# Kernel tuning notes

Measured on AMD Instinct MI355X. Metric: run time of the kernel, lower is better.

## Reference

```python
import jax, jax.numpy as jnp
import numpy as np

EPS = 1e-5

def _conv1x1(x, w, b):
    # x: [B,C,H,W], w: [O,C], b: [O]  (1x1 conv == channel matmul)
    return jnp.einsum('bchw,oc->bohw', x, w) + b[None, :, None, None]

def _bn_relu(y, gamma, beta, mean, var):
    inv = gamma / jnp.sqrt(var + EPS)
    return jax.nn.relu(y * inv[None, :, None, None] + (beta - mean * inv)[None, :, None, None])

def setup_inputs() -> dict:
    key = jax.random.key(0)
    ks = jax.random.split(key, 8)
    B, C, H, W = 8, 2048, 48, 48
    mid = C // 4  # k = 4 -> mid_ch = 512
    s_in = (2.0 / C) ** 0.5   # kaiming-like scale for 1x1 convs from C channels
    s_mid = (2.0 / mid) ** 0.5
    return {
        'x': jax.random.normal(ks[0], (B, C, H, W), jnp.float32),
        'f_w': jax.random.normal(ks[1], (mid, C), jnp.float32) * s_in,
        'f_b': jnp.zeros((mid,), jnp.float32),
        'f_gamma': jnp.ones((mid,), jnp.float32),
        'f_beta': jnp.zeros((mid,), jnp.float32),
        'f_mean': jnp.zeros((mid,), jnp.float32),
        'f_var': jnp.ones((mid,), jnp.float32),
        'g_w': jax.random.normal(ks[2], (mid, C), jnp.float32) * s_in,
        'g_b': jnp.zeros((mid,), jnp.float32),
        'g_gamma': jnp.ones((mid,), jnp.float32),
        'g_beta': jnp.zeros((mid,), jnp.float32),
        'g_mean': jnp.zeros((mid,), jnp.float32),
        'g_var': jnp.ones((mid,), jnp.float32),
        'h_w': jax.random.normal(ks[3], (mid, C), jnp.float32) * s_in,
        'h_b': jnp.zeros((mid,), jnp.float32),
        'v_w': jax.random.normal(ks[4], (C, mid), jnp.float32) * s_mid,
        'v_b': jnp.zeros((C,), jnp.float32),
    }

def reference(x, f_w, f_b, f_gamma, f_beta, f_mean, f_var,
              g_w, g_b, g_gamma, g_beta, g_mean, g_var,
              h_w, h_b, v_w, v_b):
    B, C, H, W = x.shape
    mid = f_w.shape[0]
    N = H * W
    f_x = _bn_relu(_conv1x1(x, f_w, f_b), f_gamma, f_beta, f_mean, f_var).reshape(B, mid, N)
    g_x = _bn_relu(_conv1x1(x, g_w, g_b), g_gamma, g_beta, g_mean, g_var).reshape(B, mid, N)
    h_x = _conv1x1(x, h_w, h_b).reshape(B, mid, N)
    # z = f_x^T @ g_x : [B, N, N]
    scores = jnp.einsum('bcn,bcm->bnm', f_x, g_x) * (mid ** -0.5)
    attn = jax.nn.softmax(scores, axis=-1)
    # z = attn @ h_x^T : [B, N, mid] -> [B, mid, H, W]
    z = jnp.einsum('bnm,bcm->bcn', attn, h_x).reshape(B, mid, H, W)
    z = jnp.einsum('bchw,oc->bohw', z, v_w) + v_b[None, :, None, None]
    return (z + x, attn)
```

## Files before the change

### kernel.cpp

```cpp
#include <hip/hip_runtime.h>
#include <math.h>

typedef unsigned short u16;
typedef unsigned short u16x8 __attribute__((ext_vector_type(8)));
typedef __bf16 bf16x8 __attribute__((ext_vector_type(8)));
typedef float f32x4 __attribute__((ext_vector_type(4)));

typedef __attribute__((address_space(1))) const unsigned int gu32;
typedef __attribute__((address_space(3))) unsigned int su32;

#define B_ 8
#define C_ 2048
#define MID_ 512
#define N_ 2304

#define BAR() do { asm volatile("" ::: "memory"); __builtin_amdgcn_s_barrier(); asm volatile("" ::: "memory"); } while (0)

#define QMFMA(AV, BV, MO, NO)                                                             \
  { _Pragma("unroll") for (int mfi = 0; mfi < 4; ++mfi) {                                 \
      _Pragma("unroll") for (int nfi = 0; nfi < 2; ++nfi) {                               \
        acc[MO + mfi][NO + nfi] = __builtin_amdgcn_mfma_f32_16x16x32_bf16(                \
            AV[0][mfi], BV[0][nfi], acc[MO + mfi][NO + nfi], 0, 0, 0);                    \
        acc[MO + mfi][NO + nfi] = __builtin_amdgcn_mfma_f32_16x16x32_bf16(                \
            AV[1][mfi], BV[1][nfi], acc[MO + mfi][NO + nfi], 0, 0, 0); } } }

static __device__ __forceinline__ u16 f2bf(float f) {
  union { float f; unsigned u; } c; c.f = f;
  unsigned u = c.u;
  u += 0x7fffu + ((u >> 16) & 1u);
  return (u16)(u >> 16);
}
static __device__ __forceinline__ float bf2f(u16 x) {
  union { unsigned u; float f; } c; c.u = ((unsigned)x) << 16; return c.f;
}

__global__ __launch_bounds__(256) void prep_wall_k(
    const float* __restrict__ fw, const float* __restrict__ gw,
    const float* __restrict__ hw, u16* __restrict__ wall) {
  int idx = blockIdx.x * 256 + threadIdx.x;
  if (idx >= 1536 * 2048) return;
  int r = idx >> 11;
  float v = (r < 512) ? fw[idx] : (r < 1024) ? gw[idx - (512 << 11)] : hw[idx - (1024 << 11)];
  wall[idx] = f2bf(v);
}

__global__ __launch_bounds__(256) void prep_vw_k(const float* __restrict__ vw, u16* __restrict__ o) {
  int idx = blockIdx.x * 256 + threadIdx.x;
  if (idx < 2048 * 512) o[idx] = f2bf(vw[idx]);
}

__global__ __launch_bounds__(256) void prep_sb_k(
    const float* fb, const float* fg, const float* fbe, const float* fm, const float* fv,
    const float* gb, const float* gg, const float* gbe, const float* gm, const float* gv,
    const float* hb, float* __restrict__ scale, float* __restrict__ bias) {
  int i = blockIdx.x * 256 + threadIdx.x;
  if (i >= 1536) return;
  const float FS = 0.044194173824159216f;
  if (i < 512) {
    float inv = fg[i] / sqrtf(fv[i] + 1e-5f);
    scale[i] = inv * FS; bias[i] = (fb[i] * inv + fbe[i] - fm[i] * inv) * FS;
  } else if (i < 1024) {
    int j = i - 512;
    float inv = gg[j] / sqrtf(gv[j] + 1e-5f);
    scale[i] = inv; bias[i] = gb[j] * inv + gbe[j] - gm[j] * inv;
  } else {
    scale[i] = 1.0f; bias[i] = hb[i - 1024];
  }
}

__global__ __launch_bounds__(256) void transpose_x_k(const float* __restrict__ x, u16* __restrict__ xT) {
  __shared__ float tile[64][68];
  const int b = blockIdx.z;
  const int n0 = blockIdx.x * 64, c0 = blockIdx.y * 64;
  const float* xb = x + (size_t)b * C_ * N_;
  u16* xTb = xT + (size_t)b * N_ * C_;
  const int r = threadIdx.x >> 2, q = threadIdx.x & 3;
  #pragma unroll
  for (int j = 0; j < 4; ++j) {
    float4 v = *(const float4*)&xb[(size_t)(c0 + r) * N_ + n0 + (q + 4 * j) * 4];
    *(float4*)&tile[r][(q + 4 * j) * 4] = v;
  }
  __syncthreads();
  #pragma unroll
  for (int g = 0; g < 2; ++g) {
    const int cl = (q * 2 + g) * 8;
    u16x8 w;
    #pragma unroll
    for (int e = 0; e < 8; ++e) w[e] = f2bf(tile[cl + e][r]);
    *(u16x8*)&xTb[(size_t)(n0 + r) * C_ + c0 + cl] = w;
  }
}

__global__ __launch_bounds__(256) void transpose_h_k(const u16* __restrict__ fghT, u16* __restrict__ hx) {
  __shared__ u16 tile[32][33];
  const int b = blockIdx.z;
  const int n0 = blockIdx.x * 32, c0 = blockIdx.y * 32;
  const u16* src = fghT + (size_t)b * N_ * 1536;
  u16* dst = hx + (size_t)b * MID_ * N_;
  const int tx = threadIdx.x & 31, ty = threadIdx.x >> 5;
  #pragma unroll
  for (int i = 0; i < 4; ++i)
    tile[ty + i * 8][tx] = src[(size_t)(n0 + ty + i * 8) * 1536 + 1024 + c0 + tx];
  __syncthreads();
  #pragma unroll
  for (int i = 0; i < 4; ++i)
    dst[(size_t)(c0 + ty + i * 8) * N_ + n0 + tx] = tile[tx][ty + i * 8];
}

#define EP_FG 0
#define EP_SCALE16 1
#define EP_FINAL 2

template<int EPI, int SWZ, int GX, int GY>
__global__ __launch_bounds__(512, 2) void gemm5_kernel(
    const u16* __restrict__ Ag, int lda, long long sA,
    const u16* __restrict__ Bg, int ldb, long long sB,
    void* __restrict__ Cg, int ldc, long long sC, int K,
    const float* __restrict__ ep_scale, const float* __restrict__ ep_bias,
    const float* __restrict__ ep_x, long long sX)
{
  extern __shared__ __align__(16) u16 smem[];
  u16* As = smem;
  u16* Bs = smem + 2 * 256 * 64;

  int tx, ty, tz;
  {
    const int L = blockIdx.x;
    const int xcd = L & 7, r = L >> 3;
    if constexpr (SWZ == 0) {
      const int i = r % GX, j = (r / GX) * 8 + xcd;
      tx = i; ty = j % GY; tz = j / GY;
    } else if constexpr (SWZ == 1) {
      const int i = r % GY, j = (r / GY) * 8 + xcd;
      ty = i; tx = j % GX; tz = j / GX;
    } else {
      const int i = r % 9, jg = (r / 9) * 8 + xcd;
      const int bx = jg % (GX / 3), rem = jg / (GX / 3);
      const int by = rem % (GY / 3); tz = rem / (GY / 3);
      tx = bx * 3 + i % 3; ty = by * 3 + i / 3;
    }
  }

  const int tid = threadIdx.x;
  const int lane = tid & 63;
  const int wv = tid >> 6;
  const int b = tz;
  const int m0 = ty * 256;
  const int n0 = tx * 256;
  const int wm = (wv >> 2) * 128;
  const int wn = (wv & 3) * 64;
  const int lr = lane & 15, lg = lane >> 4;

  const u16* Ab = Ag + (size_t)b * sA;
  const u16* Bb = Bg + (size_t)b * sB;
  const int nk = K >> 6;

  const int srow = lane >> 3;
  const int sksw = ((lane & 7) ^ srow) * 8;

  const int rdsw0 = ((0 + lg) ^ (lr & 7)) * 8;
  const int rdsw1 = ((4 + lg) ^ (lr & 7)) * 8;

  f32x4 acc[8][4];
  #pragma unroll
  for (int i = 0; i < 8; ++i)
    #pragma unroll
    for (int j = 0; j < 4; ++j)
      acc[i][j] = f32x4{0.f, 0.f, 0.f, 0.f};

  auto STAGE_A = [&](int p2, int t) {
    #pragma unroll
    for (int j = 0; j < 4; ++j) {
      const int rb = j * 64 + wv * 8;
      const u16* g = Ab + (size_t)(m0 + rb + srow) * lda + t * 64 + sksw;
      __builtin_amdgcn_global_load_lds((gu32*)g, (su32*)(As + p2 * 16384 + rb * 64), 16, 0, 0);
    }
  };
  auto STAGE_B = [&](int p2, int t) {
    #pragma unroll
    for (int j = 0; j < 4; ++j) {
      const int rb = j * 64 + wv * 8;
      const u16* g = Bb + (size_t)(n0 + rb + srow) * ldb + t * 64 + sksw;
      __builtin_amdgcn_global_load_lds((gu32*)g, (su32*)(Bs + p2 * 16384 + rb * 64), 16, 0, 0);
    }
  };

  STAGE_A(0, 0); STAGE_B(0, 0);
  if (nk > 1) { STAGE_A(1, 1); STAGE_B(1, 1); }

  for (int kt = 0; kt < nk; ++kt) {
    const int p = kt & 1;
    if (kt + 1 < nk) asm volatile("s_waitcnt vmcnt(8)" ::: "memory");
    else             asm volatile("s_waitcnt vmcnt(0)" ::: "memory");
    BAR();

    const u16* Asl = As + p * 16384;
    const u16* Bsl = Bs + p * 16384;
    const bool st = (kt + 2) < nk;
    const int ps = (kt + 2) & 1;

    bf16x8 aV[2][4], bLo[2][2], bHi[2][2];

    #pragma unroll
    for (int ks = 0; ks < 2; ++ks) {
      const int ro = ks ? rdsw1 : rdsw0;
      #pragma unroll
      for (int i = 0; i < 4; ++i)
        aV[ks][i] = *(const bf16x8*)(Asl + (wm + i * 16 + lr) * 64 + ro);
      #pragma unroll
      for (int i = 0; i < 2; ++i)
        bLo[ks][i] = *(const bf16x8*)(Bsl + (wn + i * 16 + lr) * 64 + ro);
    }
    BAR();
    __builtin_amdgcn_s_setprio(1);
    QMFMA(aV, bLo, 0, 0);
    __builtin_amdgcn_s_setprio(0);
    BAR();

    #pragma unroll
    for (int ks = 0; ks < 2; ++ks) {
      const int ro = ks ? rdsw1 : rdsw0;
      #pragma unroll
      for (int i = 0; i < 2; ++i)
        bHi[ks][i] = *(const bf16x8*)(Bsl + (wn + 32 + i * 16 + lr) * 64 + ro);
    }
    BAR();
    __builtin_amdgcn_s_setprio(1);
    QMFMA(aV, bHi, 0, 2);
    __builtin_amdgcn_s_setprio(0);
    BAR();

    #pragma unroll
    for (int ks = 0; ks < 2; ++ks) {
      const int ro = ks ? rdsw1 : rdsw0;
      #pragma unroll
      for (int i = 0; i < 4; ++i)
        aV[ks][i] = *(const bf16x8*)(Asl + (wm + 64 + i * 16 + lr) * 64 + ro);
    }
    if (st) STAGE_B(ps, kt + 2);
    BAR();
    __builtin_amdgcn_s_setprio(1);
    QMFMA(aV, bLo, 4, 0);
    __builtin_amdgcn_s_setprio(0);
    BAR();

    if (st) STAGE_A(ps, kt + 2);
    BAR();
    __builtin_amdgcn_s_setprio(1);
    QMFMA(aV, bHi, 4, 2);
    __builtin_amdgcn_s_setprio(0);
    BAR();
  }

  u16*   C16 = (u16*)Cg + (size_t)b * sC;
  float* C32 = (float*)Cg + (size_t)b * sC;
  const float* xb = (EPI == EP_FINAL) ? (ep_x + (size_t)b * sX) : nullptr;
  #pragma unroll
  for (int mf = 0; mf < 8; ++mf) {
    #pragma unroll
    for (int nf = 0; nf < 4; ++nf) {
      #pragma unroll
      for (int r = 0; r < 4; ++r) {
        int row = m0 + wm + mf * 16 + lg * 4 + r;
        int col = n0 + wn + nf * 16 + lr;
        float v = acc[mf][nf][r];
        if constexpr (EPI == EP_FG) {
          v = v * ep_scale[col] + ep_bias[col];
          if (col < 1024) v = fmaxf(v, 0.f);
          C16[(size_t)row * ldc + col] = f2bf(v);
        } else if constexpr (EPI == EP_SCALE16) {
          C16[(size_t)row * ldc + col] = f2bf(v);
        } else {
          v += ep_bias[row] + xb[(size_t)row * ldc + col];
          C32[(size_t)row * ldc + col] = v;
        }
      }
    }
  }
}

__global__ __launch_bounds__(256) void softmax_k(u16* __restrict__ SP, float* __restrict__ attn) {
  u16* sp = SP + (size_t)blockIdx.x * N_;
  float* ar = attn + (size_t)blockIdx.x * N_;
  const int tid = threadIdx.x;
  u16x8 s8 = *(const u16x8*)&sp[tid * 8];
  u16 st = sp[2048 + tid];
  float w[8], wt = bf2f(st);
  #pragma unroll
  for (int j = 0; j < 8; ++j) w[j] = bf2f(s8[j]);
  float mx = wt;
  #pragma unroll
  for (int j = 0; j < 8; ++j) mx = fmaxf(mx, w[j]);
  #pragma unroll
  for (int o = 32; o; o >>= 1) mx = fmaxf(mx, __shfl_xor(mx, o));
  __shared__ float red[4], red2[4];
  if ((tid & 63) == 0) red[tid >> 6] = mx;
  __syncthreads();
  mx = fmaxf(fmaxf(red[0], red[1]), fmaxf(red[2], red[3]));
  float s = 0.f;
  #pragma unroll
  for (int j = 0; j < 8; ++j) { w[j] = __expf(w[j] - mx); s += w[j]; }
  wt = __expf(wt - mx); s += wt;
  #pragma unroll
  for (int o = 32; o; o >>= 1) s += __shfl_xor(s, o);
  if ((tid & 63) == 0) red2[tid >> 6] = s;
  __syncthreads();
  s = red2[0] + red2[1] + red2[2] + red2[3];
  float inv = 1.0f / s;
  #pragma unroll
  for (int j = 0; j < 8; ++j) w[j] *= inv;
  wt *= inv;
  float4 o0 = {w[0], w[1], w[2], w[3]}, o1 = {w[4], w[5], w[6], w[7]};
  *(float4*)&ar[tid * 8] = o0;
  *(float4*)&ar[tid * 8 + 4] = o1;
  ar[2048 + tid] = wt;
  u16x8 p8;
  #pragma unroll
  for (int j = 0; j < 8; ++j) p8[j] = f2bf(w[j]);
  *(u16x8*)&sp[tid * 8] = p8;
  sp[2048 + tid] = f2bf(wt);
}

extern "C" void kernel_launch(void* const* d_in, const int* in_sizes, int n_in,
                              void* d_out, int out_size, void* d_ws, size_t ws_size,
                              hipStream_t stream) {
  const float* x    = (const float*)d_in[0];
  const float* f_w  = (const float*)d_in[1];
  const float* f_b  = (const float*)d_in[2];
  const float* f_ga = (const float*)d_in[3];
  const float* f_be = (const float*)d_in[4];
  const float* f_me = (const float*)d_in[5];
  const float* f_va = (const float*)d_in[6];
  const float* g_w  = (const float*)d_in[7];
  const float* g_b  = (const float*)d_in[8];
  const float* g_ga = (const float*)d_in[9];
  const float* g_be = (const float*)d_in[10];
  const float* g_me = (const float*)d_in[11];
  const float* g_va = (const float*)d_in[12];
  const float* h_w  = (const float*)d_in[13];
  const float* h_b  = (const float*)d_in[14];
  const float* v_w  = (const float*)d_in[15];
  const float* v_b  = (const float*)d_in[16];

  float* out0 = (float*)d_out;
  float* attn = out0 + (size_t)B_ * C_ * N_;

  char* p = (char*)d_ws;
  u16* xT   = (u16*)p; p += (size_t)B_ * N_ * C_ * 2;
  u16* fghT = (u16*)p; p += (size_t)B_ * N_ * 1536 * 2;
  u16* hx   = (u16*)p; p += (size_t)B_ * MID_ * N_ * 2;
  u16* ZT   = (u16*)p; p += (size_t)B_ * N_ * MID_ * 2;
  u16* Wall = (u16*)p; p += (size_t)1536 * C_ * 2;
  u16* vwb  = (u16*)p; p += (size_t)C_ * MID_ * 2;
  float* sc = (float*)p; p += 1536 * 4;
  float* bi = (float*)p; p += 1536 * 4;
  u16* SP   = (u16*)p; p += (size_t)B_ * N_ * N_ * 2;

  hipFuncSetAttribute((const void*)gemm5_kernel<EP_FG, 0, 6, 9>,      hipFuncAttributeMaxDynamicSharedMemorySize, 131072);
  hipFuncSetAttribute((const void*)gemm5_kernel<EP_SCALE16, 2, 9, 9>, hipFuncAttributeMaxDynamicSharedMemorySize, 131072);
  hipFuncSetAttribute((const void*)gemm5_kernel<EP_SCALE16, 0, 2, 9>, hipFuncAttributeMaxDynamicSharedMemorySize, 131072);
  hipFuncSetAttribute((const void*)gemm5_kernel<EP_FINAL, 1, 9, 8>,   hipFuncAttributeMaxDynamicSharedMemorySize, 131072);

  prep_wall_k<<<(1536 * 2048 + 255) / 256, 256, 0, stream>>>(f_w, g_w, h_w, Wall);
  prep_vw_k<<<(2048 * 512 + 255) / 256, 256, 0, stream>>>(v_w, vwb);
  prep_sb_k<<<6, 256, 0, stream>>>(f_b, f_ga, f_be, f_me, f_va,
                                   g_b, g_ga, g_be, g_me, g_va, h_b, sc, bi);
  transpose_x_k<<<dim3(N_ / 64, C_ / 64, B_), 256, 0, stream>>>(x, xT);

  gemm5_kernel<EP_FG, 0, 6, 9><<<dim3(6 * 9 * 8), 512, 131072, stream>>>(
      xT, C_, (long long)N_ * C_, Wall, C_, 0,
      fghT, 1536, (long long)N_ * 1536, C_, sc, bi, nullptr, 0);

  transpose_h_k<<<dim3(N_ / 32, MID_ / 32, B_), 256, 0, stream>>>(fghT, hx);

  gemm5_kernel<EP_SCALE16, 2, 9, 9><<<dim3(9 * 9 * 8), 512, 131072, stream>>>(
      fghT, 1536, (long long)N_ * 1536, fghT + 512, 1536, (long long)N_ * 1536,
      SP, N_, (long long)N_ * N_, MID_, nullptr, nullptr, nullptr, 0);

  softmax_k<<<B_ * N_, 256, 0, stream>>>(SP, attn);

  gemm5_kernel<EP_SCALE16, 0, 2, 9><<<dim3(2 * 9 * 8), 512, 131072, stream>>>(
      SP, N_, (long long)N_ * N_, hx, N_, (long long)MID_ * N_,
      ZT, MID_, (long long)N_ * MID_, N_, nullptr, nullptr, nullptr, 0);

  gemm5_kernel<EP_FINAL, 1, 9, 8><<<dim3(9 * 8 * 8), 512, 131072, stream>>>(
      vwb, MID_, 0, ZT, MID_, (long long)N_ * MID_,
      out0, N_, (long long)C_ * N_, MID_, nullptr, v_b, x, (long long)C_ * N_);
}
```

Before: 505.2 us.

## Run projection GEMMs and output projection in FP8 with a new fp8 MFMA kernel

Converts the input transpose, the f/g/h weights and the v weights to FP8 (e4m3) instead of bf16, and adds a gemm8 kernel that uses fp8 MFMA with half-size LDS tiles. The fgh projection and the final v projection run through it, and the attention@h GEMM now writes its output in FP8. The aim is to halve memory traffic and double MFMA throughput for the two large input-side GEMMs. The cost is a large precision loss in the K=2048 projection feeding attention scores, which may break accuracy tolerance.

```diff
diff --git a/kernel.cpp b/kernel.cpp
--- a/kernel.cpp
+++ b/kernel.cpp
@@ -1,7 +1,9 @@
 #include <hip/hip_runtime.h>
 #include <math.h>
 
+typedef unsigned char  u8;
 typedef unsigned short u16;
+typedef unsigned int   u32;
 typedef unsigned short u16x8 __attribute__((ext_vector_type(8)));
 typedef __bf16 bf16x8 __attribute__((ext_vector_type(8)));
 typedef float f32x4 __attribute__((ext_vector_type(4)));
@@ -24,6 +26,14 @@
         acc[MO + mfi][NO + nfi] = __builtin_amdgcn_mfma_f32_16x16x32_bf16(                \
             AV[1][mfi], BV[1][nfi], acc[MO + mfi][NO + nfi], 0, 0, 0); } } }
 
+#define QMFMA8(AV, BV, MO, NO)                                                            \
+  { _Pragma("unroll") for (int mfi = 0; mfi < 4; ++mfi) {                                 \
+      _Pragma("unroll") for (int nfi = 0; nfi < 2; ++nfi) {                               \
+        acc[MO + mfi][NO + nfi] = __builtin_amdgcn_mfma_f32_16x16x32_fp8_fp8(             \
+            AV[0][mfi], BV[0][nfi], acc[MO + mfi][NO + nfi], 0, 0, 0);                    \
+        acc[MO + mfi][NO + nfi] = __builtin_amdgcn_mfma_f32_16x16x32_fp8_fp8(             \
+            AV[1][mfi], BV[1][nfi], acc[MO + mfi][NO + nfi], 0, 0, 0); } } }
+
 static __device__ __forceinline__ u16 f2bf(float f) {
   union { float f; unsigned u; } c; c.f = f;
   unsigned u = c.u;
@@ -33,20 +43,29 @@
 static __device__ __forceinline__ float bf2f(u16 x) {
   union { unsigned u; float f; } c; c.u = ((unsigned)x) << 16; return c.f;
 }
-
-__global__ __launch_bounds__(256) void prep_wall_k(
+static __device__ __forceinline__ u32 pk4_fp8(float a, float b, float c, float d) {
+  u32 lo = __builtin_amdgcn_cvt_pk_fp8_f32(a, b, 0, false);
+  return __builtin_amdgcn_cvt_pk_fp8_f32(c, d, lo, true);
+}
+static __device__ __forceinline__ u8 f2fp8(float a) {
+  return (u8)(__builtin_amdgcn_cvt_pk_fp8_f32(a, a, 0, false) & 0xff);
+}
+
+__global__ __launch_bounds__(256) void prep_w8_k(
     const float* __restrict__ fw, const float* __restrict__ gw,
-    const float* __restrict__ hw, u16* __restrict__ wall) {
-  int idx = blockIdx.x * 256 + threadIdx.x;
-  if (idx >= 1536 * 2048) return;
-  int r = idx >> 11;
-  float v = (r < 512) ? fw[idx] : (r < 1024) ? gw[idx - (512 << 11)] : hw[idx - (1024 << 11)];
-  wall[idx] = f2bf(v);
-}
-
-__global__ __launch_bounds__(256) void prep_vw_k(const float* __restrict__ vw, u16* __restrict__ o) {
-  int idx = blockIdx.x * 256 + threadIdx.x;
-  if (idx < 2048 * 512) o[idx] = f2bf(vw[idx]);
+    const float* __restrict__ hw, const float* __restrict__ vw,
+    u8* __restrict__ wall8, u8* __restrict__ vw8) {
+  int w = blockIdx.x * 256 + threadIdx.x;
+  float4 v; u8* dst;
+  if (w < 786432) {
+    int e = w * 4; int r = e >> 11;
+    const float* s = (r < 512) ? (fw + e) : (r < 1024) ? (gw + e - (512 << 11)) : (hw + e - (1024 << 11));
+    v = *(const float4*)s; dst = wall8 + e;
+  } else if (w < 786432 + 262144) {
+    int e = (w - 786432) * 4;
+    v = *(const float4*)(vw + e); dst = vw8 + e;
+  } else return;
+  *(u32*)dst = pk4_fp8(v.x, v.y, v.z, v.w);
 }
 
 __global__ __launch_bounds__(256) void prep_sb_k(
@@ -68,12 +87,12 @@
   }
 }
 
-__global__ __launch_bounds__(256) void transpose_x_k(const float* __restrict__ x, u16* __restrict__ xT) {
+__global__ __launch_bounds__(256) void transpose_x_k(const float* __restrict__ x, u8* __restrict__ xT) {
   __shared__ float tile[64][68];
   const int b = blockIdx.z;
   const int n0 = blockIdx.x * 64, c0 = blockIdx.y * 64;
   const float* xb = x + (size_t)b * C_ * N_;
-  u16* xTb = xT + (size_t)b * N_ * C_;
+  u8* xTb = xT + (size_t)b * N_ * C_;
   const int r = threadIdx.x >> 2, q = threadIdx.x & 3;
   #pragma unroll
   for (int j = 0; j < 4; ++j) {
@@ -84,10 +103,10 @@
   #pragma unroll
   for (int g = 0; g < 2; ++g) {
     const int cl = (q * 2 + g) * 8;
-    u16x8 w;
-    #pragma unroll
-    for (int e = 0; e < 8; ++e) w[e] = f2bf(tile[cl + e][r]);
-    *(u16x8*)&xTb[(size_t)(n0 + r) * C_ + c0 + cl] = w;
+    uint2 w;
+    w.x = pk4_fp8(tile[cl + 0][r], tile[cl + 1][r], tile[cl + 2][r], tile[cl + 3][r]);
+    w.y = pk4_fp8(tile[cl + 4][r], tile[cl + 5][r], tile[cl + 6][r], tile[cl + 7][r]);
+    *(uint2*)&xTb[(size_t)(n0 + r) * C_ + c0 + cl] = w;
   }
 }
 
@@ -110,6 +129,7 @@
 #define EP_FG 0
 #define EP_SCALE16 1
 #define EP_FINAL 2
+#define EP_FP8 3
 
 template<int EPI, int SWZ, int GX, int GY>
 __global__ __launch_bounds__(512, 2) void gemm5_kernel(
@@ -157,7 +177,6 @@
 
   const int srow = lane >> 3;
   const int sksw = ((lane & 7) ^ srow) * 8;
-
   const int rdsw0 = ((0 + lg) ^ (lr & 7)) * 8;
   const int rdsw1 = ((4 + lg) ^ (lr & 7)) * 8;
 
@@ -254,6 +273,7 @@
 
   u16*   C16 = (u16*)Cg + (size_t)b * sC;
   float* C32 = (float*)Cg + (size_t)b * sC;
+  u8*    C8  = (u8*)Cg  + (size_t)b * sC;
   const float* xb = (EPI == EP_FINAL) ? (ep_x + (size_t)b * sX) : nullptr;
   #pragma unroll
   for (int mf = 0; mf < 8; ++mf) {
@@ -269,6 +289,167 @@
           if (col < 1024) v = fmaxf(v, 0.f);
           C16[(size_t)row * ldc + col] = f2bf(v);
         } else if constexpr (EPI == EP_SCALE16) {
+          C16[(size_t)row * ldc + col] = f2bf(v);
+        } else if constexpr (EPI == EP_FP8) {
+          C8[(size_t)row * ldc + col] = f2fp8(v);
+        } else {
+          v += ep_bias[row] + xb[(size_t)row * ldc + col];
+          C32[(size_t)row * ldc + col] = v;
+        }
+      }
+    }
+  }
+}
+
+template<int EPI, int SWZ, int GX, int GY>
+__global__ __launch_bounds__(512, 2) void gemm8_kernel(
+    const u8* __restrict__ Ag, int lda, long long sA,
+    const u8* __restrict__ Bg, int ldb, long long sB,
+    void* __restrict__ Cg, int ldc, long long sC, int K,
+    const float* __restrict__ ep_scale, const float* __restrict__ ep_bias,
+    const float* __restrict__ ep_x, long long sX)
+{
+  extern __shared__ __align__(16) u8 smem8[];
+  u8* As = smem8;
+  u8* Bs = smem8 + 2 * 256 * 64;
+
+  int tx, ty, tz;
+  {
+    const int L = blockIdx.x;
+    const int xcd = L & 7, r = L >> 3;
+    if constexpr (SWZ == 0) {
+      const int i = r % GX, j = (r / GX) * 8 + xcd;
+      tx = i; ty = j % GY; tz = j / GY;
+    } else {
+      const int i = r % GY, j = (r / GY) * 8 + xcd;
+      ty = i; tx = j % GX; tz = j / GX;
+    }
+  }
+
+  const int tid = threadIdx.x;
+  const int lane = tid & 63;
+  const int wv = tid >> 6;
+  const int b = tz;
+  const int m0 = ty * 256;
+  const int n0 = tx * 256;
+  const int wm = (wv >> 2) * 128;
+  const int wn = (wv & 3) * 64;
+  const int lr = lane & 15, lg = lane >> 4;
+
+  const u8* Ab = Ag + (size_t)b * sA;
+  const u8* Bb = Bg + (size_t)b * sB;
+  const int nk = K >> 6;
+
+  const int s16row = lane >> 2;
+  const int schunk = ((lane & 3) ^ (s16row & 3)) * 16;
+  const int oA = (lg ^ ((lr & 3) << 1)) * 8;
+
+  f32x4 acc[8][4];
+  #pragma unroll
+  for (int i = 0; i < 8; ++i)
+    #pragma unroll
+    for (int j = 0; j < 4; ++j)
+      acc[i][j] = f32x4{0.f, 0.f, 0.f, 0.f};
+
+  auto STAGE_A = [&](int p2, int t) {
+    #pragma unroll
+    for (int j = 0; j < 2; ++j) {
+      const int rb = j * 128 + wv * 16;
+      const u8* g = Ab + (size_t)(m0 + rb + s16row) * lda + t * 64 + schunk;
+      __builtin_amdgcn_global_load_lds((gu32*)g, (su32*)(As + p2 * 16384 + rb * 64), 16, 0, 0);
+    }
+  };
+  auto STAGE_B = [&](int p2, int t) {
+    #pragma unroll
+    for (int j = 0; j < 2; ++j) {
+      const int rb = j * 128 + wv * 16;
+      const u8* g = Bb + (size_t)(n0 + rb + s16row) * ldb + t * 64 + schunk;
+      __builtin_amdgcn_global_load_lds((gu32*)g, (su32*)(Bs + p2 * 16384 + rb * 64), 16, 0, 0);
+    }
+  };
+
+  STAGE_A(0, 0); STAGE_B(0, 0);
+  if (nk > 1) { STAGE_A(1, 1); STAGE_B(1, 1); }
+
+  for (int kt = 0; kt < nk; ++kt) {
+    const int p = kt & 1;
+    if (kt + 1 < nk) asm volatile("s_waitcnt vmcnt(4)" ::: "memory");
+    else             asm volatile("s_waitcnt vmcnt(0)" ::: "memory");
+    BAR();
+
+    const u8* Asl = As + p * 16384;
+    const u8* Bsl = Bs + p * 16384;
+    const bool st = (kt + 2) < nk;
+    const int ps = (kt + 2) & 1;
+
+    long aV[2][4], bLo[2][2], bHi[2][2];
+
+    #pragma unroll
+    for (int ks = 0; ks < 2; ++ks) {
+      const int ro = oA ^ (ks * 32);
+      #pragma unroll
+      for (int i = 0; i < 4; ++i)
+        aV[ks][i] = *(const long*)(Asl + (wm + i * 16 + lr) * 64 + ro);
+      #pragma unroll
+      for (int i = 0; i < 2; ++i)
+        bLo[ks][i] = *(const long*)(Bsl + (wn + i * 16 + lr) * 64 + ro);
+    }
+    BAR();
+    __builtin_amdgcn_s_setprio(1);
+    QMFMA8(aV, bLo, 0, 0);
+    __builtin_amdgcn_s_setprio(0);
+    BAR();
+
+    #pragma unroll
+    for (int ks = 0; ks < 2; ++ks) {
+      const int ro = oA ^ (ks * 32);
+      #pragma unroll
+      for (int i = 0; i < 2; ++i)
+        bHi[ks][i] = *(const long*)(Bsl + (wn + 32 + i * 16 + lr) * 64 + ro);
+    }
+    BAR();
+    __builtin_amdgcn_s_setprio(1);
+    QMFMA8(aV, bHi, 0, 2);
+    __builtin_amdgcn_s_setprio(0);
+    BAR();
+
+    #pragma unroll
+    for (int ks = 0; ks < 2; ++ks) {
+      const int ro = oA ^ (ks * 32);
+      #pragma unroll
+      for (int i = 0; i < 4; ++i)
+        aV[ks][i] = *(const long*)(Asl + (wm + 64 + i * 16 + lr) * 64 + ro);
+    }
+    if (st) STAGE_B(ps, kt + 2);
+    BAR();
+    __builtin_amdgcn_s_setprio(1);
+    QMFMA8(aV, bLo, 4, 0);
+    __builtin_amdgcn_s_setprio(0);
+    BAR();
+
+    if (st) STAGE_A(ps, kt + 2);
+    BAR();
+    __builtin_amdgcn_s_setprio(1);
+    QMFMA8(aV, bHi, 4, 2);
+    __builtin_amdgcn_s_setprio(0);
+    BAR();
+  }
+
+  u16*   C16 = (u16*)Cg + (size_t)b * sC;
+  float* C32 = (float*)Cg + (size_t)b * sC;
+  const float* xb = (EPI == EP_FINAL) ? (ep_x + (size_t)b * sX) : nullptr;
+  #pragma unroll
+  for (int mf = 0; mf < 8; ++mf) {
+    #pragma unroll
+    for (int nf = 0; nf < 4; ++nf) {
+      #pragma unroll
+      for (int r = 0; r < 4; ++r) {
+        int row = m0 + wm + mf * 16 + lg * 4 + r;
+        int col = n0 + wn + nf * 16 + lr;
+        float v = acc[mf][nf][r];
+        if constexpr (EPI == EP_FG) {
+          v = v * ep_scale[col] + ep_bias[col];
+          if (col < 1024) v = fmaxf(v, 0.f);
           C16[(size_t)row * ldc + col] = f2bf(v);
         } else {
           v += ep_bias[row] + xb[(size_t)row * ldc + col];
@@ -346,29 +527,29 @@
   float* attn = out0 + (size_t)B_ * C_ * N_;
 
   char* p = (char*)d_ws;
-  u16* xT   = (u16*)p; p += (size_t)B_ * N_ * C_ * 2;
+  u8*  xT8  = (u8*)p;  p += (size_t)B_ * N_ * C_;
   u16* fghT = (u16*)p; p += (size_t)B_ * N_ * 1536 * 2;
   u16* hx   = (u16*)p; p += (size_t)B_ * MID_ * N_ * 2;
-  u16* ZT   = (u16*)p; p += (size_t)B_ * N_ * MID_ * 2;
-  u16* Wall = (u16*)p; p += (size_t)1536 * C_ * 2;
-  u16* vwb  = (u16*)p; p += (size_t)C_ * MID_ * 2;
+  u8*  ZT8  = (u8*)p;  p += (size_t)B_ * N_ * MID_;
+  u8*  Wall8= (u8*)p;  p += (size_t)1536 * C_;
+  u8*  vwb8 = (u8*)p;  p += (size_t)C_ * MID_;
   float* sc = (float*)p; p += 1536 * 4;
   float* bi = (float*)p; p += 1536 * 4;
+  p = (char*)(((size_t)p + 255) & ~(size_t)255);
   u16* SP   = (u16*)p; p += (size_t)B_ * N_ * N_ * 2;
 
-  hipFuncSetAttribute((const void*)gemm5_kernel<EP_FG, 0, 6, 9>,      hipFuncAttributeMaxDynamicSharedMemorySize, 131072);
   hipFuncSetAttribute((const void*)gemm5_kernel<EP_SCALE16, 2, 9, 9>, hipFuncAttributeMaxDynamicSharedMemorySize, 131072);
-  hipFuncSetAttribute((const void*)gemm5_kernel<EP_SCALE16, 0, 2, 9>, hipFuncAttributeMaxDynamicSharedMemorySize, 131072);
-  hipFuncSetAttribute((const void*)gemm5_kernel<EP_FINAL, 1, 9, 8>,   hipFuncAttributeMaxDynamicSharedMemorySize, 131072);
-
-  prep_wall_k<<<(1536 * 2048 + 255) / 256, 256, 0, stream>>>(f_w, g_w, h_w, Wall);
-  prep_vw_k<<<(2048 * 512 + 255) / 256, 256, 0, stream>>>(v_w, vwb);
+  hipFuncSetAttribute((const void*)gemm5_kernel<EP_FP8, 0, 2, 9>,     hipFuncAttributeMaxDynamicSharedMemorySize, 131072);
+  hipFuncSetAttribute((const void*)gemm8_kernel<EP_FG, 0, 6, 9>,      hipFuncAttributeMaxDynamicSharedMemorySize, 65536);
+  hipFuncSetAttribute((const void*)gemm8_kernel<EP_FINAL, 1, 9, 8>,   hipFuncAttributeMaxDynamicSharedMemorySize, 65536);
+
+  prep_w8_k<<<(786432 + 262144 + 255) / 256, 256, 0, stream>>>(f_w, g_w, h_w, v_w, Wall8, vwb8);
   prep_sb_k<<<6, 256, 0, stream>>>(f_b, f_ga, f_be, f_me, f_va,
                                    g_b, g_ga, g_be, g_me, g_va, h_b, sc, bi);
-  transpose_x_k<<<dim3(N_ / 64, C_ / 64, B_), 256, 0, stream>>>(x, xT);
-
-  gemm5_kernel<EP_FG, 0, 6, 9><<<dim3(6 * 9 * 8), 512, 131072, stream>>>(
-      xT, C_, (long long)N_ * C_, Wall, C_, 0,
+  transpose_x_k<<<dim3(N_ / 64, C_ / 64, B_), 256, 0, stream>>>(x, xT8);
+
+  gemm8_kernel<EP_FG, 0, 6, 9><<<dim3(6 * 9 * 8), 512, 65536, stream>>>(
+      xT8, C_, (long long)N_ * C_, Wall8, C_, 0,
       fghT, 1536, (long long)N_ * 1536, C_, sc, bi, nullptr, 0);
 
   transpose_h_k<<<dim3(N_ / 32, MID_ / 32, B_), 256, 0, stream>>>(fghT, hx);
@@ -379,11 +560,11 @@
 
   softmax_k<<<B_ * N_, 256, 0, stream>>>(SP, attn);
 
-  gemm5_kernel<EP_SCALE16, 0, 2, 9><<<dim3(2 * 9 * 8), 512, 131072, stream>>>(
+  gemm5_kernel<EP_FP8, 0, 2, 9><<<dim3(2 * 9 * 8), 512, 131072, stream>>>(
       SP, N_, (long long)N_ * N_, hx, N_, (long long)MID_ * N_,
-      ZT, MID_, (long long)N_ * MID_, N_, nullptr, nullptr, nullptr, 0);
-
-  gemm5_kernel<EP_FINAL, 1, 9, 8><<<dim3(9 * 8 * 8), 512, 131072, stream>>>(
-      vwb, MID_, 0, ZT, MID_, (long long)N_ * MID_,
+      ZT8, MID_, (long long)N_ * MID_, N_, nullptr, nullptr, nullptr, 0);
+
+  gemm8_kernel<EP_FINAL, 1, 9, 8><<<dim3(9 * 8 * 8), 512, 65536, stream>>>(
+      vwb8, MID_, 0, ZT8, MID_, (long long)N_ * MID_,
       out0, N_, (long long)C_ * N_, MID_, nullptr, v_b, x, (long long)C_ * N_);
 }
```

Result: slower. 531.7 us (+5.2%).
